# Kernel tuning notes

Hardware: AMD Instinct MI355X
Metric: run time of the kernel (lower is better)

## Reference

```python
import jax, jax.numpy as jnp
import numpy as np
import math

EPS = 1.1920929e-07  # torch.finfo(float32).eps, used by nn.RMSNorm(eps=None)

def rmsnorm(x, w):
    return x * jax.lax.rsqrt(jnp.mean(x * x, axis=-1, keepdims=True) + EPS) * w

def sinkhorn(logits, iters=20):
    m = jnp.exp(logits - logits.max(axis=-1, keepdims=True))
    def body(_, m):
        m = m / (m.sum(axis=-1, keepdims=True) + 1e-6)
        return m / (m.sum(axis=-2, keepdims=True) + 1e-6)
    return jax.lax.fori_loop(0, iters, body, m)

def ngram_hash(ids, mults):
    # ids [B,T] int32, mults [2,2,3] int32 -> [B,T,4]
    B, T = ids.shape
    padded = jnp.pad(ids, ((0, 0), (2, 0)))
    windows = jnp.stack([padded[:, k:k + T] for k in range(3)], axis=-1)  # [B,T,3]
    out = []
    for n_idx in range(2):
        L = n_idx + 2
        grams = windows[:, :, 3 - L:]                                     # [B,T,L]
        mixed = grams[:, :, None, :] * mults[n_idx, :, :L][None, None]    # [B,T,2,L]
        h = mixed[..., 0]
        for k in range(1, L):
            h = jnp.bitwise_xor(h, mixed[..., k])
        out.append(h % 4096)
    return jnp.concatenate(out, axis=2)

def short_conv(x, conv_w, norm_w):
    # depthwise causal conv, kernel 4: torch pads 3 both sides then slices [..., :T]
    B, T, G, C = x.shape
    xn = rmsnorm(x, norm_w).reshape(B, T, G * C).transpose(0, 2, 1)  # [B,GC,T]
    y = jax.lax.conv_general_dilated(xn, conv_w, (1,), [(3, 0)],
                                     feature_group_count=G * C,
                                     dimension_numbers=('NCH', 'OIH', 'NCH'))
    return jax.nn.silu(y).transpose(0, 2, 1).reshape(B, T, G, C)

def engram(x, ids, mults, emb_table, val_w, val_b, key_w, key_b, nq_w, nk_w, conv_w, convnorm_w):
    B, T = ids.shape
    hash_ids = ngram_hash(ids, mults) + jnp.array([0, 4096, 8192, 12288], dtype=jnp.int32)
    emb = emb_table[hash_ids].reshape(B, T, -1)                       # [B,T,256]
    v_base = emb @ val_w + val_b                                      # [B,T,128]
    k = rmsnorm(jnp.einsum('btd,sdc->btsc', emb, key_w) + key_b, nk_w)  # [B,T,4,128]
    q = rmsnorm(x, nq_w)
    gates = jax.nn.sigmoid(jnp.sum(q * k, axis=-1, keepdims=True) / math.sqrt(128.0))
    v_gated = v_base[:, :, None, :] * gates                           # [B,T,4,128]
    return v_gated + short_conv(v_gated, conv_w, convnorm_w)

def causal_attn(x, qkv_w, qkv_b, proj_w, proj_b):
    B, T, C = x.shape
    H, D = 4, C // 4
    q, k, v = jnp.split(x @ qkv_w + qkv_b, 3, axis=-1)
    q = q.reshape(B, T, H, D).transpose(0, 2, 1, 3)
    k = k.reshape(B, T, H, D).transpose(0, 2, 1, 3)
    v = v.reshape(B, T, H, D).transpose(0, 2, 1, 3)
    att = jnp.einsum('bhtd,bhsd->bhts', q, k) / math.sqrt(D)
    att = jnp.where(jnp.tril(jnp.ones((T, T), bool)), att, -jnp.inf)
    att = jax.nn.softmax(att, axis=-1)
    y = jnp.einsum('bhts,bhsd->bhtd', att, v).transpose(0, 2, 1, 3).reshape(B, T, C)
    return y @ proj_w + proj_b

def mhc(x, layer_fn, coef_w, pre_w, pre_b, post_w, post_b, res_w, res_b, a_pre, a_post, a_res, ln_w):
    B, T, n, C = x.shape
    xn = rmsnorm(x.reshape(B * T, n * C), coef_w)
    H_pre = jax.nn.sigmoid(a_pre * (xn @ pre_w + pre_b))             # [BT,n]
    H_post = 2.0 * jax.nn.sigmoid(a_post * (xn @ post_w + post_b))   # [BT,n]
    H_res = sinkhorn((a_res * (xn @ res_w + res_b)).reshape(-1, n, n))
    xp = x.reshape(B * T, n, C)
    x_agg = jnp.einsum('bn,bnc->bc', H_pre, xp)
    y = layer_fn(rmsnorm(x_agg.reshape(B, T, C), ln_w)).reshape(B * T, C)
    # faithful to torch einsum 'bjn,bc->bnc' applied to H_post.transpose(1,2) [BT,n,1]:
    # the stream dim j is CONTRACTED, leaving a size-1 dim that broadcasts over streams
    x_branch = H_post.sum(axis=-1)[:, None, None] * y[:, None, :]    # [BT,1,C]
    x_highway = jnp.einsum('bnm,bmc->bnc', H_res, xp)                # [BT,n,C]
    return (x_highway + x_branch).reshape(B, T, n, C)

def _forward(x, input_ids, eng_multipliers, eng_embedding, eng_val_w, eng_val_b, eng_key_w, eng_key_b, eng_nq_w, eng_nk_w, eng_conv_w, eng_convnorm_w, a_coef_w, a_pre_w, a_pre_b, a_post_w, a_post_b, a_res_w, a_res_b, a_alpha_pre, a_alpha_post, a_alpha_res, a_ln_w, qkv_w, qkv_b, attnproj_w, attnproj_b, m_coef_w, m_pre_w, m_pre_b, m_post_w, m_post_b, m_res_w, m_res_b, m_alpha_pre, m_alpha_post, m_alpha_res, m_ln_w, mlp_w1, mlp_b1, mlp_w2, mlp_b2):
    x = x + engram(x, input_ids, eng_multipliers, eng_embedding, eng_val_w, eng_val_b, eng_key_w, eng_key_b, eng_nq_w, eng_nk_w, eng_conv_w, eng_convnorm_w)
    attn_fn = lambda z: causal_attn(z, qkv_w, qkv_b, attnproj_w, attnproj_b)
    x = mhc(x, attn_fn, a_coef_w, a_pre_w, a_pre_b, a_post_w, a_post_b, a_res_w, a_res_b, a_alpha_pre, a_alpha_post, a_alpha_res, a_ln_w)
    mlp_fn = lambda z: jax.nn.silu(z @ mlp_w1 + mlp_b1) @ mlp_w2 + mlp_b2
    x = mhc(x, mlp_fn, m_coef_w, m_pre_w, m_pre_b, m_post_w, m_post_b, m_res_w, m_res_b, m_alpha_pre, m_alpha_post, m_alpha_res, m_ln_w)
    return x

def setup_inputs():
    key = jax.random.key(0)
    B, T = 256, 128
    def rnd(i, shp, scale=0.02):
        return jax.random.normal(jax.random.fold_in(key, i), shp, jnp.float32) * scale
    alpha = jnp.asarray(0.01, jnp.float32)
    return {
        'x': rnd(0, (B, T, 4, 128), 1.0),
        'input_ids': jax.random.randint(jax.random.fold_in(key, 1), (B, T), 0, 4096, jnp.int32),
        'eng_multipliers': jax.random.randint(jax.random.fold_in(key, 2), (2, 2, 3), 1, 10000, jnp.int32),
        'eng_embedding': rnd(3, (16384, 64)),
        'eng_val_w': rnd(4, (256, 128)), 'eng_val_b': jnp.zeros(128, jnp.float32),
        'eng_key_w': rnd(5, (4, 256, 128)), 'eng_key_b': jnp.zeros((4, 128), jnp.float32),
        'eng_nq_w': jnp.ones((4, 128), jnp.float32), 'eng_nk_w': jnp.ones((4, 128), jnp.float32),
        'eng_conv_w': rnd(6, (512, 1, 4), 0.1), 'eng_convnorm_w': jnp.ones((4, 128), jnp.float32),
        'a_coef_w': jnp.ones(512, jnp.float32),
        'a_pre_w': rnd(7, (512, 4)), 'a_pre_b': jnp.zeros(4, jnp.float32),
        'a_post_w': rnd(8, (512, 4)), 'a_post_b': jnp.zeros(4, jnp.float32),
        'a_res_w': rnd(9, (512, 16)), 'a_res_b': jnp.zeros(16, jnp.float32),
        'a_alpha_pre': alpha, 'a_alpha_post': alpha, 'a_alpha_res': alpha,
        'a_ln_w': jnp.ones(128, jnp.float32),
        'qkv_w': rnd(10, (128, 384)), 'qkv_b': jnp.zeros(384, jnp.float32),
        'attnproj_w': rnd(11, (128, 128)), 'attnproj_b': jnp.zeros(128, jnp.float32),
        'm_coef_w': jnp.ones(512, jnp.float32),
        'm_pre_w': rnd(12, (512, 4)), 'm_pre_b': jnp.zeros(4, jnp.float32),
        'm_post_w': rnd(13, (512, 4)), 'm_post_b': jnp.zeros(4, jnp.float32),
        'm_res_w': rnd(14, (512, 16)), 'm_res_b': jnp.zeros(16, jnp.float32),
        'm_alpha_pre': alpha, 'm_alpha_post': alpha, 'm_alpha_res': alpha,
        'm_ln_w': jnp.ones(128, jnp.float32),
        'mlp_w1': rnd(15, (128, 512)), 'mlp_b1': jnp.zeros(512, jnp.float32),
        'mlp_w2': rnd(16, (512, 128)), 'mlp_b2': jnp.zeros(128, jnp.float32),
    }

def reference(x, input_ids, eng_multipliers, eng_embedding, eng_val_w, eng_val_b, eng_key_w, eng_key_b, eng_nq_w, eng_nk_w, eng_conv_w, eng_convnorm_w, a_coef_w, a_pre_w, a_pre_b, a_post_w, a_post_b, a_res_w, a_res_b, a_alpha_pre, a_alpha_post, a_alpha_res, a_ln_w, qkv_w, qkv_b, attnproj_w, attnproj_b, m_coef_w, m_pre_w, m_pre_b, m_post_w, m_post_b, m_res_w, m_res_b, m_alpha_pre, m_alpha_post, m_alpha_res, m_ln_w, mlp_w1, mlp_b1, mlp_w2, mlp_b2):
    return _forward(x, input_ids, eng_multipliers, eng_embedding, eng_val_w, eng_val_b, eng_key_w, eng_key_b, eng_nq_w, eng_nk_w, eng_conv_w, eng_convnorm_w, a_coef_w, a_pre_w, a_pre_b, a_post_w, a_post_b, a_res_w, a_res_b, a_alpha_pre, a_alpha_post, a_alpha_res, a_ln_w, qkv_w, qkv_b, attnproj_w, attnproj_b, m_coef_w, m_pre_w, m_pre_b, m_post_w, m_post_b, m_res_w, m_res_b, m_alpha_pre, m_alpha_post, m_alpha_res, m_ln_w, mlp_w1, mlp_b1, mlp_w2, mlp_b2)
```

## Files before the change

kernel.cpp:

```cpp
#include <hip/hip_runtime.h>

#define BT 32768
#define TSEQ 128

constexpr float EPSF = 1.1920929e-07f;

typedef __attribute__((ext_vector_type(8))) short bf16x8;
typedef __attribute__((ext_vector_type(4))) float f32x4;

__device__ __forceinline__ float sigm(float z) { return 1.f / (1.f + __expf(-z)); }

__device__ __forceinline__ short bf16c(float f) {
  union { float f; unsigned u; } v; v.f = f;
  unsigned r = v.u + 0x7FFFu + ((v.u >> 16) & 1u);
  return (short)(r >> 16);
}
__device__ __forceinline__ float bf2f(short s) {
  union { unsigned u; float f; } v; v.u = ((unsigned)(unsigned short)s) << 16;
  return v.f;
}

__device__ __forceinline__ float red64(float v) {
  v += __shfl_xor(v, 1);  v += __shfl_xor(v, 2);  v += __shfl_xor(v, 4);
  v += __shfl_xor(v, 8);  v += __shfl_xor(v, 16); v += __shfl_xor(v, 32);
  return v;
}
__device__ __forceinline__ float red32(float v) {
  v += __shfl_xor(v, 1); v += __shfl_xor(v, 2); v += __shfl_xor(v, 4);
  v += __shfl_xor(v, 8); v += __shfl_xor(v, 16);
  return v;
}
__device__ __forceinline__ float red16(float v) {
  v += __shfl_xor(v, 1); v += __shfl_xor(v, 2); v += __shfl_xor(v, 4); v += __shfl_xor(v, 8);
  return v;
}
__device__ __forceinline__ float redmax16(float v) {
  v = fmaxf(v, __shfl_xor(v, 1)); v = fmaxf(v, __shfl_xor(v, 2));
  v = fmaxf(v, __shfl_xor(v, 4)); v = fmaxf(v, __shfl_xor(v, 8));
  return v;
}
__device__ __forceinline__ void load8(float* d, const float* p) {
  const float4 a = *reinterpret_cast<const float4*>(p);
  const float4 b = *reinterpret_cast<const float4*>(p + 4);
  d[0]=a.x; d[1]=a.y; d[2]=a.z; d[3]=a.w; d[4]=b.x; d[5]=b.y; d[6]=b.z; d[7]=b.w;
}

__global__ __launch_bounds__(256) void prep(
    const float* __restrict__ qkv_w, const float* __restrict__ proj_w,
    const float* __restrict__ mlp_w1, const float* __restrict__ mlp_w2,
    const float* __restrict__ val_w, const float* __restrict__ key_w,
    const float* __restrict__ a_res_w, const float* __restrict__ a_pre_w,
    const float* __restrict__ a_post_w,
    const float* __restrict__ m_res_w, const float* __restrict__ m_pre_w,
    const float* __restrict__ m_post_w,
    const float* __restrict__ a_res_b, const float* __restrict__ a_pre_b,
    const float* __restrict__ a_post_b,
    const float* __restrict__ m_res_b, const float* __restrict__ m_pre_b,
    const float* __restrict__ m_post_b,
    short* __restrict__ wt_qkv, short* __restrict__ wt_proj,
    short* __restrict__ wt_mlp1, short* __restrict__ wt_mlp2,
    short* __restrict__ wt_eng, short* __restrict__ wpk_a,
    short* __restrict__ wpk_m, float* __restrict__ bpk_a,
    float* __restrict__ bpk_m)
{
  const int idx = blockIdx.x * 256 + threadIdx.x;
  if (idx < 49152) {
    const int n = idx >> 7, k = idx & 127;
    wt_qkv[idx] = bf16c(qkv_w[k * 384 + n]);
  } else if (idx < 65536) {
    const int j = idx - 49152; const int n = j >> 7, k = j & 127;
    wt_proj[j] = bf16c(proj_w[k * 128 + n]);
  } else if (idx < 131072) {
    const int j = idx - 65536; const int n = j >> 7, k = j & 127;
    wt_mlp1[j] = bf16c(mlp_w1[k * 512 + n]);
  } else if (idx < 196608) {
    const int j = idx - 131072; const int n = j >> 9, k = j & 511;
    wt_mlp2[j] = bf16c(mlp_w2[k * 128 + n]);
  } else if (idx < 360448) {
    const int j = idx - 196608; const int n = j >> 8, k = j & 255;
    float v;
    if (n < 128) v = val_w[k * 128 + n];
    else v = key_w[(size_t)((n - 128) >> 7) * 32768 + k * 128 + (n & 127)];
    wt_eng[j] = bf16c(v);
  } else if (idx < 376832) {
    const int j = idx - 360448; const int r = j >> 9, k = j & 511;
    float v = 0.f;
    if (r < 16) v = a_res_w[k * 16 + r];
    else if (r < 20) v = a_pre_w[k * 4 + (r - 16)];
    else if (r < 24) v = a_post_w[k * 4 + (r - 20)];
    wpk_a[j] = bf16c(v);
  } else if (idx < 393216) {
    const int j = idx - 376832; const int r = j >> 9, k = j & 511;
    float v = 0.f;
    if (r < 16) v = m_res_w[k * 16 + r];
    else if (r < 20) v = m_pre_w[k * 4 + (r - 16)];
    else if (r < 24) v = m_post_w[k * 4 + (r - 20)];
    wpk_m[j] = bf16c(v);
  } else if (idx < 393280) {
    const int j = idx - 393216;
    if (j < 32) {
      float v = 0.f;
      if (j < 16) v = a_res_b[j];
      else if (j < 20) v = a_pre_b[j - 16];
      else if (j < 24) v = a_post_b[j - 20];
      bpk_a[j] = v;
    } else {
      const int r = j - 32;
      float v = 0.f;
      if (r < 16) v = m_res_b[r];
      else if (r < 20) v = m_pre_b[r - 16];
      else if (r < 24) v = m_post_b[r - 20];
      bpk_m[r] = v;
    }
  }
}

__global__ __launch_bounds__(256) void mgemm32(
    const unsigned short* __restrict__ Ab, const int lda,
    const short* __restrict__ WT, const float* __restrict__ bias,
    float* __restrict__ out, const int K,
    const float* __restrict__ rinv, const float* __restrict__ csc)
{
  __shared__ short As[64 * 64];
  __shared__ short Bs[32 * 64];
  const int tid = threadIdx.x;
  const int i0 = blockIdx.x * 64;
  const int w = tid >> 6, l = tid & 63;
  const int wm = w >> 1, wn = w & 1;
  const int kg = l >> 4, lr = l & 15;
  f32x4 acc[2];
  acc[0] = {0.f, 0.f, 0.f, 0.f};
  acc[1] = {0.f, 0.f, 0.f, 0.f};

  for (int kc = 0; kc < K; kc += 64) {
    __syncthreads();
#pragma unroll
    for (int p = 0; p < 2; ++p) {
      const int idx = p * 256 + tid;
      const int r = idx >> 3, ko = idx & 7;
      const bf16x8 v = *reinterpret_cast<const bf16x8*>(Ab + (size_t)(i0 + r) * lda + kc + ko * 8);
      const float rs = rinv[i0 + r];
      const float4 ca = *reinterpret_cast<const float4*>(csc + kc + ko * 8);
      const float4 cb = *reinterpret_cast<const float4*>(csc + kc + ko * 8 + 4);
      bf16x8 o;
      o[0] = bf16c(bf2f(v[0]) * rs * ca.x);
      o[1] = bf16c(bf2f(v[1]) * rs * ca.y);
      o[2] = bf16c(bf2f(v[2]) * rs * ca.z);
      o[3] = bf16c(bf2f(v[3]) * rs * ca.w);
      o[4] = bf16c(bf2f(v[4]) * rs * cb.x);
      o[5] = bf16c(bf2f(v[5]) * rs * cb.y);
      o[6] = bf16c(bf2f(v[6]) * rs * cb.z);
      o[7] = bf16c(bf2f(v[7]) * rs * cb.w);
      *reinterpret_cast<bf16x8*>(&As[r * 64 + ((ko ^ (r & 7)) << 3)]) = o;
    }
    {
      const int r = tid >> 3, slb = tid & 7;
      const bf16x8 v = *reinterpret_cast<const bf16x8*>(WT + (size_t)r * K + kc + slb * 8);
      *reinterpret_cast<bf16x8*>(&Bs[r * 64 + ((slb ^ (r & 7)) << 3)]) = v;
    }
    __syncthreads();
#pragma unroll
    for (int ks = 0; ks < 2; ++ks) {
      const int slot = ks * 4 + kg;
      bf16x8 af[2], bft;
#pragma unroll
      for (int mi = 0; mi < 2; ++mi) {
        const int r = wm * 32 + mi * 16 + lr;
        af[mi] = *reinterpret_cast<const bf16x8*>(&As[r * 64 + ((slot ^ (r & 7)) << 3)]);
      }
      {
        const int rb = wn * 16 + lr;
        bft = *reinterpret_cast<const bf16x8*>(&Bs[rb * 64 + ((slot ^ (rb & 7)) << 3)]);
      }
#pragma unroll
      for (int mi = 0; mi < 2; ++mi)
        acc[mi] = __builtin_amdgcn_mfma_f32_16x16x32_bf16(af[mi], bft, acc[mi], 0, 0, 0);
    }
  }
#pragma unroll
  for (int mi = 0; mi < 2; ++mi) {
    const int col = wn * 16 + lr;
    const float bv = bias[col];
#pragma unroll
    for (int j = 0; j < 4; ++j) {
      const int row = i0 + wm * 32 + mi * 16 + kg * 4 + j;
      out[(size_t)row * 32 + col] = acc[mi][j] + bv;
    }
  }
}

__global__ __launch_bounds__(256) void eng_mgemm(
    const int* __restrict__ ids, const int* __restrict__ mults,
    const float* __restrict__ table, const float* __restrict__ val_b,
    const short* __restrict__ wt_eng,
    float* __restrict__ vbase, unsigned short* __restrict__ krawb)
{
  __shared__ int hid[128][4];
  __shared__ short As[128 * 64];
  __shared__ short Bs[128 * 64];
  const int tid = threadIdx.x;
  const int i0 = blockIdx.x * 128;
  const int by = blockIdx.y;
  const int c0 = by * 128;
#pragma unroll
  for (int p = 0; p < 2; ++p) {
    const int idx = tid + p * 256;
    const int r = idx >> 2, wh = idx & 3;
    const int i = i0 + r;
    const int b = i >> 7, tt = i & 127;
    const int* __restrict__ row = ids + b * TSEQ;
    const int g2 = row[tt];
    const int g1 = (tt >= 1) ? row[tt - 1] : 0;
    const int g0 = (tt >= 2) ? row[tt - 2] : 0;
    int h;
    if (wh == 0)      h = ((g1 * mults[0]) ^ (g2 * mults[1])) & 4095;
    else if (wh == 1) h = (((g1 * mults[3]) ^ (g2 * mults[4])) & 4095) + 4096;
    else if (wh == 2) h = (((g0 * mults[6]) ^ (g1 * mults[7]) ^ (g2 * mults[8])) & 4095) + 8192;
    else              h = (((g0 * mults[9]) ^ (g1 * mults[10]) ^ (g2 * mults[11])) & 4095) + 12288;
    hid[r][wh] = h;
  }
  const int w = tid >> 6, l = tid & 63;
  const int wr = (w >> 1) * 64, wc = (w & 1) * 64;
  f32x4 acc[4][4];
#pragma unroll
  for (int mi = 0; mi < 4; ++mi)
#pragma unroll
    for (int ni = 0; ni < 4; ++ni) acc[mi][ni] = {0.f, 0.f, 0.f, 0.f};

  const int c4 = tid & 15;
  const int asl = c4 >> 1, ahf = c4 & 1;
  const int bsl = tid & 7;

  for (int kc = 0; kc < 256; kc += 64) {
    const int seg = kc >> 6;
    __syncthreads();
#pragma unroll
    for (int p = 0; p < 8; ++p) {
      const int r = (tid >> 4) + p * 16;
      const float4 v = *reinterpret_cast<const float4*>(table + (size_t)hid[r][seg] * 64 + c4 * 4);
      short4 b4; b4.x = bf16c(v.x); b4.y = bf16c(v.y); b4.z = bf16c(v.z); b4.w = bf16c(v.w);
      *reinterpret_cast<short4*>(&As[r * 64 + ((asl ^ (r & 7)) << 3) + (ahf << 2)]) = b4;
    }
#pragma unroll
    for (int p = 0; p < 4; ++p) {
      const int r = (tid >> 3) + p * 32;
      const bf16x8 v = *reinterpret_cast<const bf16x8*>(wt_eng + (size_t)(c0 + r) * 256 + kc + bsl * 8);
      *reinterpret_cast<bf16x8*>(&Bs[r * 64 + ((bsl ^ (r & 7)) << 3)]) = v;
    }
    __syncthreads();
    const int kg = l >> 4, lr = l & 15;
#pragma unroll
    for (int ks = 0; ks < 2; ++ks) {
      const int slot = ks * 4 + kg;
      bf16x8 af[4], bft[4];
#pragma unroll
      for (int mi = 0; mi < 4; ++mi) {
        const int r = wr + mi * 16 + lr;
        af[mi] = *reinterpret_cast<const bf16x8*>(&As[r * 64 + ((slot ^ (r & 7)) << 3)]);
      }
#pragma unroll
      for (int ni = 0; ni < 4; ++ni) {
        const int r = wc + ni * 16 + lr;
        bft[ni] = *reinterpret_cast<const bf16x8*>(&Bs[r * 64 + ((slot ^ (r & 7)) << 3)]);
      }
#pragma unroll
      for (int mi = 0; mi < 4; ++mi)
#pragma unroll
        for (int ni = 0; ni < 4; ++ni)
          acc[mi][ni] = __builtin_amdgcn_mfma_f32_16x16x32_bf16(af[mi], bft[ni], acc[mi][ni], 0, 0, 0);
    }
  }
  const int lr = l & 15, hi = l >> 4;
#pragma unroll
  for (int mi = 0; mi < 4; ++mi)
#pragma unroll
    for (int ni = 0; ni < 4; ++ni) {
      const int col = wc + ni * 16 + lr;
#pragma unroll
      for (int j = 0; j < 4; ++j) {
        const int row = i0 + wr + mi * 16 + hi * 4 + j;
        if (by == 0)
          vbase[(size_t)row * 128 + col] = acc[mi][ni][j] + val_b[col];
        else
          krawb[(size_t)row * 512 + (by - 1) * 128 + col] =
              (unsigned short)bf16c(acc[mi][ni][j]);
      }
    }
}

__global__ __launch_bounds__(256) void fused_gateconv(
    const unsigned short* __restrict__ krawb, const float* __restrict__ x,
    const float* __restrict__ vbase, const float* __restrict__ key_b,
    const float* __restrict__ nk_w, const float* __restrict__ nq_w,
    const float* __restrict__ conv_w, const float* __restrict__ cnw,
    unsigned short* __restrict__ xout, float* __restrict__ invout)
{
  __shared__ float vb[19 * 128];
  __shared__ float gA[19][4];
  __shared__ float gG[19][4];
  const int tid = threadIdx.x;
  const size_t rowbase = (size_t)blockIdx.x * 16;
  const int tt0 = (int)(rowbase & 127);
#pragma unroll
  for (int p = 0; p < 3; ++p) {
    const int idx = p * 256 + tid;
    if (idx < 608) {
      const int hs = idx >> 5, c4 = (idx & 31) << 2;
      float4 v = make_float4(0.f, 0.f, 0.f, 0.f);
      if (tt0 - 3 + hs >= 0)
        v = *reinterpret_cast<const float4*>(vbase + (rowbase - 3 + hs) * 128 + c4);
      *reinterpret_cast<float4*>(&vb[hs * 128 + c4]) = v;
    }
  }
  __syncthreads();
  const int w = tid >> 6, l = tid & 63;
  {
    const int s = l >> 4, li = l & 15, c0 = li * 8, j0 = l * 8;
    float kb[8], nk[8], nq[8];
    load8(kb, key_b + s * 128 + c0);
    load8(nk, nk_w + s * 128 + c0);
    load8(nq, nq_w + s * 128 + c0);
    for (int it = 0; it < 5; ++it) {
      const int ht = it * 4 + w;
      if (ht >= 19) break;
      const int tt = tt0 - 3 + ht;
      if (tt < 0) {
        if (li == 0) { gG[ht][s] = 0.f; gA[ht][s] = 0.f; }
        continue;
      }
      const size_t rg = rowbase - 3 + ht;
      float kv[8], xv[8];
      {
        const bf16x8 kvb = *reinterpret_cast<const bf16x8*>(krawb + rg * 512 + j0);
#pragma unroll
        for (int jj = 0; jj < 8; ++jj) kv[jj] = bf2f(kvb[jj]);
      }
      load8(xv, x + rg * 512 + j0);
      float ssk = 0.f, ssx = 0.f;
#pragma unroll
      for (int jj = 0; jj < 8; ++jj) {
        kv[jj] += kb[jj];
        ssk = fmaf(kv[jj], kv[jj], ssk);
        ssx = fmaf(xv[jj], xv[jj], ssx);
      }
      ssk = red16(ssk);
      ssx = red16(ssx);
      const float invk = rsqrtf(ssk * (1.f / 128.f) + EPSF);
      const float invq = rsqrtf(ssx * (1.f / 128.f) + EPSF);
      float dot = 0.f;
#pragma unroll
      for (int jj = 0; jj < 8; ++jj)
        dot = fmaf(kv[jj] * invk * nk[jj], xv[jj] * invq * nq[jj], dot);
      dot = red16(dot);
      const float gate = sigm(dot * 0.08838834764831843f);
      const float2 vb2 = *reinterpret_cast<const float2*>(&vb[ht * 128 + l * 2]);
      float ssv = vb2.x * vb2.x + vb2.y * vb2.y;
      ssv = red64(ssv);
      const float A = gate * rsqrtf(gate * gate * (ssv * (1.f / 128.f)) + EPSF);
      if (li == 0) { gG[ht][s] = gate; gA[ht][s] = A; }
    }
  }
  __syncthreads();
  {
    const int tg = tid >> 5;
    const int c4l = tid & 31;
    const int cf = c4l * 4;
    for (int ti = 0; ti < 2; ++ti) {
      const int t = tg + ti * 8;
      const size_t rg = rowbase + t;
      float ssq = 0.f;
#pragma unroll
      for (int sj = 0; sj < 4; ++sj) {
        const int j = sj * 128 + cf;
        float4 cwe[4];
#pragma unroll
        for (int e = 0; e < 4; ++e)
          cwe[e] = *reinterpret_cast<const float4*>(conv_w + (size_t)(j + e) * 4);
        const float4 cn4 = *reinterpret_cast<const float4*>(cnw + j);
        float4 vbt[4]; float av[4];
#pragma unroll
        for (int kk = 0; kk < 4; ++kk) {
          vbt[kk] = *reinterpret_cast<const float4*>(&vb[(t + kk) * 128 + cf]);
          av[kk] = gA[t + kk][sj];
        }
        const float gg = gG[t + 3][sj];
        float4 accv;
        accv.x = vbt[0].x*av[0]*cwe[0].x + vbt[1].x*av[1]*cwe[0].y + vbt[2].x*av[2]*cwe[0].z + vbt[3].x*av[3]*cwe[0].w;
        accv.y = vbt[0].y*av[0]*cwe[1].x + vbt[1].y*av[1]*cwe[1].y + vbt[2].y*av[2]*cwe[1].z + vbt[3].y*av[3]*cwe[1].w;
        accv.z = vbt[0].z*av[0]*cwe[2].x + vbt[1].z*av[1]*cwe[2].y + vbt[2].z*av[2]*cwe[2].z + vbt[3].z*av[3]*cwe[2].w;
        accv.w = vbt[0].w*av[0]*cwe[3].x + vbt[1].w*av[1]*cwe[3].y + vbt[2].w*av[2]*cwe[3].z + vbt[3].w*av[3]*cwe[3].w;
        const float4 x4 = *reinterpret_cast<const float4*>(x + rg * 512 + j);
        const float y0 = accv.x * cn4.x, y1 = accv.y * cn4.y;
        const float y2 = accv.z * cn4.z, y3 = accv.w * cn4.w;
        float4 o;
        o.x = x4.x + vbt[3].x * gg + y0 * sigm(y0);
        o.y = x4.y + vbt[3].y * gg + y1 * sigm(y1);
        o.z = x4.z + vbt[3].z * gg + y2 * sigm(y2);
        o.w = x4.w + vbt[3].w * gg + y3 * sigm(y3);
        ushort4 ob;
        ob.x = (unsigned short)bf16c(o.x);
        ob.y = (unsigned short)bf16c(o.y);
        ob.z = (unsigned short)bf16c(o.z);
        ob.w = (unsigned short)bf16c(o.w);
        *reinterpret_cast<ushort4*>(xout + rg * 512 + j) = ob;
        ssq += o.x*o.x + o.y*o.y + o.z*o.z + o.w*o.w;
      }
      ssq = red32(ssq);
      if (c4l == 0) invout[rg] = rsqrtf(ssq * (1.f / 512.f) + EPSF);
    }
  }
}

__global__ __launch_bounds__(256) void mhc_sink2(
    const float* __restrict__ proj, const unsigned short* __restrict__ xin,
    const float* __restrict__ p_apre, const float* __restrict__ p_apost,
    const float* __restrict__ p_ares, const float* __restrict__ ln_w,
    unsigned short* __restrict__ xab, float* __restrict__ hres,
    float* __restrict__ hps)
{
  const int tid = threadIdx.x;
  const int l = tid & 63;
  const size_t i = (size_t)blockIdx.x * 4 + (tid >> 6);
  const float pv = proj[i * 32 + (l & 31)];
  const float apre = p_apre[0], apost = p_apost[0], ares = p_ares[0];
  const int n = l >> 4;
  const float hp = sigm(apre * __shfl(pv, 16 + n));
  float hsum = 0.f;
#pragma unroll
  for (int t2 = 0; t2 < 4; ++t2) hsum += 2.f * sigm(apost * __shfl(pv, 20 + t2));
  const float v = ares * pv;
  float rm = fmaxf(v, __shfl_xor(v, 1));
  rm = fmaxf(rm, __shfl_xor(rm, 2));
  float m = __expf(v - rm);
#pragma unroll
  for (int it = 0; it < 20; ++it) {
    float rs = m + __shfl_xor(m, 1);
    rs += __shfl_xor(rs, 2);
    m *= __builtin_amdgcn_rcpf(rs + 1e-6f);
    float cs = m + __shfl_xor(m, 4);
    cs += __shfl_xor(cs, 8);
    m *= __builtin_amdgcn_rcpf(cs + 1e-6f);
  }
  if (l < 16) hres[i * 16 + l] = m;
  if (l == 0) hps[i] = hsum;
  const int j0 = l * 8;
  float xv[8];
  {
    const bf16x8 xb = *reinterpret_cast<const bf16x8*>(xin + i * 512 + j0);
#pragma unroll
    for (int jj = 0; jj < 8; ++jj) xv[jj] = bf2f(xb[jj]);
  }
  float ag[8];
#pragma unroll
  for (int jj = 0; jj < 8; ++jj) {
    float a2 = hp * xv[jj];
    a2 += __shfl_xor(a2, 16);
    a2 += __shfl_xor(a2, 32);
    ag[jj] = a2;
  }
  float ssa = 0.f;
#pragma unroll
  for (int jj = 0; jj < 8; ++jj) ssa = fmaf(ag[jj], ag[jj], ssa);
  ssa = red16(ssa);
  const float inva = rsqrtf(ssa * (1.f / 128.f) + EPSF);
  if (l < 16) {
    float lnw[8];
    load8(lnw, ln_w + l * 8);
    bf16x8 o;
#pragma unroll
    for (int jj = 0; jj < 8; ++jj) o[jj] = bf16c(ag[jj] * inva * lnw[jj]);
    *reinterpret_cast<bf16x8*>(xab + i * 128 + l * 8) = o;
  }
}

template <int NT, int ACT>
__global__ __launch_bounds__(256) void mgemm_bf16A(
    const unsigned short* __restrict__ Ab, const short* __restrict__ WT,
    const float* __restrict__ bias, unsigned short* __restrict__ outp)
{
  __shared__ short As[128 * 64];
  __shared__ short Bs[128 * 64];
  const int tid = threadIdx.x;
  const int i0 = blockIdx.x * 128;
  const int c0 = blockIdx.y * 128;
  const int w = tid >> 6, l = tid & 63;
  const int wr = (w >> 1) * 64, wc = (w & 1) * 64;
  const int kg = l >> 4, lr = l & 15;
  f32x4 acc[4][4];
#pragma unroll
  for (int mi = 0; mi < 4; ++mi)
#pragma unroll
    for (int ni = 0; ni < 4; ++ni) acc[mi][ni] = {0.f, 0.f, 0.f, 0.f};

#pragma unroll
  for (int kc = 0; kc < 2; ++kc) {
    __syncthreads();
#pragma unroll
    for (int p = 0; p < 4; ++p) {
      const int idx = p * 256 + tid;
      const int r = idx >> 3, slb = idx & 7;
      const bf16x8 v = *reinterpret_cast<const bf16x8*>(Ab + (size_t)(i0 + r) * 128 + kc * 64 + slb * 8);
      *reinterpret_cast<bf16x8*>(&As[r * 64 + ((slb ^ (r & 7)) << 3)]) = v;
    }
#pragma unroll
    for (int p = 0; p < 4; ++p) {
      const int idx = p * 256 + tid;
      const int r = idx >> 3, slb = idx & 7;
      const bf16x8 v = *reinterpret_cast<const bf16x8*>(WT + (size_t)(c0 + r) * 128 + kc * 64 + slb * 8);
      *reinterpret_cast<bf16x8*>(&Bs[r * 64 + ((slb ^ (r & 7)) << 3)]) = v;
    }
    __syncthreads();
#pragma unroll
    for (int ks = 0; ks < 2; ++ks) {
      const int slot = ks * 4 + kg;
      bf16x8 af[4], bft[4];
#pragma unroll
      for (int mi = 0; mi < 4; ++mi) {
        const int r = wr + mi * 16 + lr;
        af[mi] = *reinterpret_cast<const bf16x8*>(&As[r * 64 + ((slot ^ (r & 7)) << 3)]);
      }
#pragma unroll
      for (int ni = 0; ni < 4; ++ni) {
        const int r = wc + ni * 16 + lr;
        bft[ni] = *reinterpret_cast<const bf16x8*>(&Bs[r * 64 + ((slot ^ (r & 7)) << 3)]);
      }
#pragma unroll
      for (int mi = 0; mi < 4; ++mi)
#pragma unroll
        for (int ni = 0; ni < 4; ++ni)
          acc[mi][ni] = __builtin_amdgcn_mfma_f32_16x16x32_bf16(af[mi], bft[ni], acc[mi][ni], 0, 0, 0);
    }
  }
#pragma unroll
  for (int mi = 0; mi < 4; ++mi)
#pragma unroll
    for (int ni = 0; ni < 4; ++ni) {
      const int col = c0 + wc + ni * 16 + lr;
      const float bv = bias[col];
#pragma unroll
      for (int j = 0; j < 4; ++j) {
        const int row = i0 + wr + mi * 16 + kg * 4 + j;
        float o = acc[mi][ni][j] + bv;
        if (ACT == 1) o = o * sigm(o);
        outp[(size_t)row * (NT * 128) + col] = (unsigned short)bf16c(o);
      }
    }
}

template <int KT, bool WITH_INV, bool OUTBF>
__global__ __launch_bounds__(512) void gemm_combine(
    const unsigned short* __restrict__ Ab, const int lda,
    const short* __restrict__ WT, const float* __restrict__ bias,
    const unsigned short* __restrict__ xst, const float* __restrict__ hres,
    const float* __restrict__ hps, void* __restrict__ outp,
    float* __restrict__ invout)
{
  __shared__ short As[64 * 64];
  __shared__ short Bs[128 * 64];
  __shared__ short yl[64 * 132];
  __shared__ float prt[64][2];
  const int tid = threadIdx.x;
  const size_t i0 = (size_t)blockIdx.x * 64;
  const int w = tid >> 6, l = tid & 63;
  const int wm = w >> 2, wn = w & 3;
  const int kg = l >> 4, lr = l & 15;
  f32x4 acc[2][2];
#pragma unroll
  for (int mi = 0; mi < 2; ++mi)
#pragma unroll
    for (int ni = 0; ni < 2; ++ni) acc[mi][ni] = {0.f, 0.f, 0.f, 0.f};
#pragma unroll
  for (int kc = 0; kc < KT; ++kc) {
    __syncthreads();
    {
      const int r = tid >> 3, slb = tid & 7;
      const bf16x8 v = *reinterpret_cast<const bf16x8*>(Ab + (i0 + r) * lda + kc * 64 + slb * 8);
      *reinterpret_cast<bf16x8*>(&As[r * 64 + ((slb ^ (r & 7)) << 3)]) = v;
    }
#pragma unroll
    for (int p = 0; p < 2; ++p) {
      const int idx = p * 512 + tid;
      const int r = idx >> 3, slb = idx & 7;
      const bf16x8 v = *reinterpret_cast<const bf16x8*>(
          WT + (size_t)r * (KT * 64) + kc * 64 + slb * 8);
      *reinterpret_cast<bf16x8*>(&Bs[r * 64 + ((slb ^ (r & 7)) << 3)]) = v;
    }
    __syncthreads();
#pragma unroll
    for (int ks = 0; ks < 2; ++ks) {
      const int slot = ks * 4 + kg;
      bf16x8 af[2], bft[2];
#pragma unroll
      for (int mi = 0; mi < 2; ++mi) {
        const int r = wm * 32 + mi * 16 + lr;
        af[mi] = *reinterpret_cast<const bf16x8*>(&As[r * 64 + ((slot ^ (r & 7)) << 3)]);
      }
#pragma unroll
      for (int ni = 0; ni < 2; ++ni) {
        const int rb = wn * 32 + ni * 16 + lr;
        bft[ni] = *reinterpret_cast<const bf16x8*>(&Bs[rb * 64 + ((slot ^ (rb & 7)) << 3)]);
      }
#pragma unroll
      for (int mi = 0; mi < 2; ++mi)
#pragma unroll
        for (int ni = 0; ni < 2; ++ni)
          acc[mi][ni] = __builtin_amdgcn_mfma_f32_16x16x32_bf16(af[mi], bft[ni], acc[mi][ni], 0, 0, 0);
    }
  }
#pragma unroll
  for (int mi = 0; mi < 2; ++mi)
#pragma unroll
    for (int ni = 0; ni < 2; ++ni) {
      const int col = wn * 32 + ni * 16 + lr;
      const float bv = bias[col];
#pragma unroll
      for (int j = 0; j < 4; ++j) {
        const int row = wm * 32 + mi * 16 + kg * 4 + j;
        yl[row * 132 + col] = bf16c(acc[mi][ni][j] + bv);
      }
    }
  __syncthreads();
  const int c = tid & 127, tl = tid >> 7;
  for (int k = 0; k < 16; ++k) {
    const int t = tl * 16 + k;
    const size_t rg = i0 + t;
    float hv[16];
#pragma unroll
    for (int n16 = 0; n16 < 16; ++n16) hv[n16] = hres[rg * 16 + n16];
    const float g = hps[rg];
    const float yv = bf2f(yl[t * 132 + c]) * g;
    float xm[4];
#pragma unroll
    for (int m = 0; m < 4; ++m) xm[m] = bf2f((short)xst[rg * 512 + m * 128 + c]);
    float ssq = 0.f;
#pragma unroll
    for (int n = 0; n < 4; ++n) {
      const float o = hv[n*4+0]*xm[0] + hv[n*4+1]*xm[1] + hv[n*4+2]*xm[2] + hv[n*4+3]*xm[3] + yv;
      if (OUTBF)
        ((unsigned short*)outp)[rg * 512 + n * 128 + c] = (unsigned short)bf16c(o);
      else
        ((float*)outp)[rg * 512 + n * 128 + c] = o;
      if (WITH_INV) ssq = fmaf(o, o, ssq);
    }
    if (WITH_INV) {
      ssq = red64(ssq);
      if (l == 0) prt[t][(tid >> 6) & 1] = ssq;
    }
  }
  if (WITH_INV) {
    __syncthreads();
    if (tid < 64)
      invout[i0 + tid] = rsqrtf((prt[tid][0] + prt[tid][1]) * (1.f / 512.f) + EPSF);
  }
}

__global__ __launch_bounds__(256) void attn_mfma(
    const unsigned short* __restrict__ qkv, unsigned short* __restrict__ y)
{
  __shared__ short Ks[128 * 32];
  __shared__ short Vt[32 * 128];
  __shared__ short Ps[4][32 * 128];
  const int tid = threadIdx.x;
  const int b = blockIdx.x >> 2, h = blockIdx.x & 3;
  const unsigned short* __restrict__ base = qkv + (size_t)b * 128 * 384 + h * 32;
#pragma unroll
  for (int p = 0; p < 2; ++p) {
    const int idx = tid + p * 256;
    const int s = idx >> 2, c8 = idx & 3;
    const bf16x8 v = *reinterpret_cast<const bf16x8*>(base + (size_t)s * 384 + 128 + c8 * 8);
    const int chunk = c8 ^ ((s >> 1) & 3);
    *reinterpret_cast<bf16x8*>(&Ks[s * 32 + chunk * 8]) = v;
  }
#pragma unroll
  for (int p = 0; p < 4; ++p) {
    const int idx = tid + p * 256;
    const int s = idx >> 3, c4 = idx & 7;
    const ushort4 v = *reinterpret_cast<const ushort4*>(base + (size_t)s * 384 + 256 + c4 * 4);
    const int schunk = s >> 3, soff = s & 7;
#pragma unroll
    for (int k = 0; k < 4; ++k) {
      const int d = c4 * 4 + k;
      const unsigned short vv = (k == 0) ? v.x : (k == 1) ? v.y : (k == 2) ? v.z : v.w;
      Vt[d * 128 + ((schunk ^ (d & 7)) << 3) + soff] = (short)vv;
    }
  }
  const int w = tid >> 6, l = tid & 63;
  const int g = l >> 4, lr = l & 15;
  bf16x8 qa[2];
#pragma unroll
  for (int mi = 0; mi < 2; ++mi) {
    const int row = w * 32 + mi * 16 + lr;
    qa[mi] = *reinterpret_cast<const bf16x8*>(base + (size_t)row * 384 + g * 8);
  }
  __syncthreads();
  const int ntmax = 2 * w + 1;
  bf16x8 ka[8];
#pragma unroll
  for (int nt = 0; nt < 8; ++nt)
    if (nt <= ntmax) {
      const int s = nt * 16 + lr;
      const int chunk = g ^ ((s >> 1) & 3);
      ka[nt] = *reinterpret_cast<const bf16x8*>(&Ks[s * 32 + chunk * 8]);
    }
  f32x4 sacc[2][8];
#pragma unroll
  for (int mi = 0; mi < 2; ++mi)
#pragma unroll
    for (int nt = 0; nt < 8; ++nt) sacc[mi][nt] = {0.f, 0.f, 0.f, 0.f};
#pragma unroll
  for (int mi = 0; mi < 2; ++mi)
#pragma unroll
    for (int nt = 0; nt < 8; ++nt)
      if (nt <= ntmax)
        sacc[mi][nt] = __builtin_amdgcn_mfma_f32_16x16x32_bf16(qa[mi], ka[nt], sacc[mi][nt], 0, 0, 0);
  const float scl = 0.17677669529663687f;
  float rv[2][4];
  short* const pw = Ps[w];
#pragma unroll
  for (int mi = 0; mi < 2; ++mi) {
#pragma unroll
    for (int j = 0; j < 4; ++j) {
      const int row = w * 32 + mi * 16 + g * 4 + j;
      float mx = -3.4e38f;
#pragma unroll
      for (int nt = 0; nt < 8; ++nt)
        if (nt <= ntmax) {
          const int col = nt * 16 + lr;
          const float val = sacc[mi][nt][j] * scl;
          if (col <= row) mx = fmaxf(mx, val);
        }
      mx = redmax16(mx);
      float sum = 0.f;
      const int rl = mi * 16 + g * 4 + j;
#pragma unroll
      for (int nt = 0; nt < 8; ++nt)
        if (nt <= ntmax) {
          const int col = nt * 16 + lr;
          const float val = sacc[mi][nt][j] * scl;
          const float pv = (col <= row) ? __expf(val - mx) : 0.f;
          sum += pv;
          const int chunk = (2 * nt + (lr >> 3)) ^ (rl & 7);
          pw[rl * 128 + chunk * 8 + (lr & 7)] = bf16c(pv);
        }
      sum = red16(sum);
      rv[mi][j] = 1.f / sum;
    }
  }
  f32x4 oacc[2][2];
#pragma unroll
  for (int mi = 0; mi < 2; ++mi)
#pragma unroll
    for (int nt = 0; nt < 2; ++nt) oacc[mi][nt] = {0.f, 0.f, 0.f, 0.f};
#pragma unroll
  for (int kt = 0; kt < 4; ++kt)
    if (kt <= w) {
      bf16x8 pa[2], va[2];
#pragma unroll
      for (int mi = 0; mi < 2; ++mi) {
        const int rl = mi * 16 + lr;
        const int chunk = (4 * kt + g) ^ (rl & 7);
        pa[mi] = *reinterpret_cast<const bf16x8*>(&pw[rl * 128 + chunk * 8]);
      }
#pragma unroll
      for (int nt = 0; nt < 2; ++nt) {
        const int d = nt * 16 + lr;
        const int chunk = (4 * kt + g) ^ (d & 7);
        va[nt] = *reinterpret_cast<const bf16x8*>(&Vt[d * 128 + chunk * 8]);
      }
#pragma unroll
      for (int mi = 0; mi < 2; ++mi)
#pragma unroll
        for (int nt = 0; nt < 2; ++nt)
          oacc[mi][nt] = __builtin_amdgcn_mfma_f32_16x16x32_bf16(pa[mi], va[nt], oacc[mi][nt], 0, 0, 0);
    }
#pragma unroll
  for (int mi = 0; mi < 2; ++mi)
#pragma unroll
    for (int nt = 0; nt < 2; ++nt)
#pragma unroll
      for (int j = 0; j < 4; ++j) {
        const int row = w * 32 + mi * 16 + g * 4 + j;
        y[((size_t)b * 128 + row) * 128 + h * 32 + nt * 16 + lr] =
            (unsigned short)bf16c(oacc[mi][nt][j] * rv[mi][j]);
      }
}

extern "C" void kernel_launch(void* const* d_in, const int* in_sizes, int n_in,
                              void* d_out, int out_size, void* d_ws, size_t ws_size,
                              hipStream_t stream)
{
  const float* x        = (const float*)d_in[0];
  const int*   ids      = (const int*)d_in[1];
  const int*   mults    = (const int*)d_in[2];
  const float* table    = (const float*)d_in[3];
  const float* val_w    = (const float*)d_in[4];
  const float* val_b    = (const float*)d_in[5];
  const float* key_w    = (const float*)d_in[6];
  const float* key_b    = (const float*)d_in[7];
  const float* nq_w     = (const float*)d_in[8];
  const float* nk_w     = (const float*)d_in[9];
  const float* conv_w   = (const float*)d_in[10];
  const float* cnw      = (const float*)d_in[11];
  const float* a_coef   = (const float*)d_in[12];
  const float* a_pre_w  = (const float*)d_in[13];
  const float* a_pre_b  = (const float*)d_in[14];
  const float* a_post_w = (const float*)d_in[15];
  const float* a_post_b = (const float*)d_in[16];
  const float* a_res_w  = (const float*)d_in[17];
  const float* a_res_b  = (const float*)d_in[18];
  const float* a_apre   = (const float*)d_in[19];
  const float* a_apost  = (const float*)d_in[20];
  const float* a_ares   = (const float*)d_in[21];
  const float* a_ln_w   = (const float*)d_in[22];
  const float* qkv_w    = (const float*)d_in[23];
  const float* qkv_b    = (const float*)d_in[24];
  const float* proj_w   = (const float*)d_in[25];
  const float* proj_b   = (const float*)d_in[26];
  const float* m_coef   = (const float*)d_in[27];
  const float* m_pre_w  = (const float*)d_in[28];
  const float* m_pre_b  = (const float*)d_in[29];
  const float* m_post_w = (const float*)d_in[30];
  const float* m_post_b = (const float*)d_in[31];
  const float* m_res_w  = (const float*)d_in[32];
  const float* m_res_b  = (const float*)d_in[33];
  const float* m_apre   = (const float*)d_in[34];
  const float* m_apost  = (const float*)d_in[35];
  const float* m_ares   = (const float*)d_in[36];
  const float* m_ln_w   = (const float*)d_in[37];
  const float* mlp_w1   = (const float*)d_in[38];
  const float* mlp_b1   = (const float*)d_in[39];
  const float* mlp_w2   = (const float*)d_in[40];
  const float* mlp_b2   = (const float*)d_in[41];

  float* out = (float*)d_out;
  float* ws  = (float*)d_ws;
  float* vbase  = ws;
  float* proj24 = vbase + (size_t)BT * 128;
  float* hresb  = proj24 + (size_t)BT * 32;
  float* hpsb   = hresb + (size_t)BT * 16;
  float* inv1   = hpsb + (size_t)BT;
  float* inv2   = inv1 + (size_t)BT;
  float* bpk_a  = inv2 + (size_t)BT;
  float* bpk_m  = bpk_a + 32;
  short* wt_qkv  = (short*)(bpk_m + 32);
  short* wt_proj = wt_qkv  + 49152;
  short* wt_mlp1 = wt_proj + 16384;
  short* wt_mlp2 = wt_mlp1 + 65536;
  short* wt_eng  = wt_mlp2 + 65536;
  short* wpk_a   = wt_eng  + 163840;
  short* wpk_m   = wpk_a   + 16384;
  unsigned short* xab = (unsigned short*)(wpk_m + 16384);
  unsigned short* big = xab + (size_t)BT * 128;
  unsigned short* x1b = big + (size_t)BT * 512;
  unsigned short* x2b = x1b + (size_t)BT * 512;
  unsigned short* y1b = xab;

  prep<<<1537, 256, 0, stream>>>(qkv_w, proj_w, mlp_w1, mlp_w2, val_w, key_w,
                                 a_res_w, a_pre_w, a_post_w, m_res_w, m_pre_w, m_post_w,
                                 a_res_b, a_pre_b, a_post_b, m_res_b, m_pre_b, m_post_b,
                                 wt_qkv, wt_proj, wt_mlp1, wt_mlp2, wt_eng,
                                 wpk_a, wpk_m, bpk_a, bpk_m);

  eng_mgemm<<<dim3(BT / 128, 5), 256, 0, stream>>>(ids, mults, table, val_b, wt_eng,
                                                   vbase, big);
  fused_gateconv<<<BT / 16, 256, 0, stream>>>(big, x, vbase, key_b, nk_w, nq_w,
                                              conv_w, cnw, x1b, inv1);

  mgemm32<<<BT / 64, 256, 0, stream>>>(x1b, 512, wpk_a, bpk_a, proj24, 512, inv1, a_coef);
  mhc_sink2<<<BT / 4, 256, 0, stream>>>(proj24, x1b, a_apre, a_apost, a_ares, a_ln_w,
                                        xab, hresb, hpsb);
  mgemm_bf16A<3, 0><<<dim3(BT / 128, 3), 256, 0, stream>>>(xab, wt_qkv, qkv_b, big);
  attn_mfma<<<1024, 256, 0, stream>>>(big, y1b);
  gemm_combine<2, true, true><<<BT / 64, 512, 0, stream>>>(
      y1b, 128, wt_proj, proj_b, x1b, hresb, hpsb, (void*)x2b, inv2);

  mgemm32<<<BT / 64, 256, 0, stream>>>(x2b, 512, wpk_m, bpk_m, proj24, 512, inv2, m_coef);
  mhc_sink2<<<BT / 4, 256, 0, stream>>>(proj24, x2b, m_apre, m_apost, m_ares, m_ln_w,
                                        xab, hresb, hpsb);
  mgemm_bf16A<4, 1><<<dim3(BT / 128, 4), 256, 0, stream>>>(xab, wt_mlp1, mlp_b1, big);
  gemm_combine<8, false, false><<<BT / 64, 512, 0, stream>>>(
      big, 512, wt_mlp2, mlp_b2, x2b, hresb, hpsb, (void*)out, nullptr);

  (void)in_sizes; (void)n_in; (void)out_size; (void)ws_size;
}
```

Before: 290.8 us.

## Pre-convert embedding table to bf16, rebalance gate loop, stage hres in LDS

The embedding table is converted to bf16 once in the prep kernel, so eng_mgemm gathers 16-byte bf16 rows instead of converting fp32 float4 loads on every tile. The fused gate/conv kernel now assigns four lanes per (row, stream) and processes four rows per wave, so the loop runs two iterations instead of five. It pays for this by reloading krawb, x and the bias vectors a second time. gemm_combine stages the hres and hps coefficients in shared memory instead of reading them per thread from global memory. The prep launch grows to cover about one million extra table elements each call.

```diff
diff --git a/kernel.cpp b/kernel.cpp
--- a/kernel.cpp
+++ b/kernel.cpp
@@ -34,6 +34,10 @@
   v += __shfl_xor(v, 1); v += __shfl_xor(v, 2); v += __shfl_xor(v, 4); v += __shfl_xor(v, 8);
   return v;
 }
+__device__ __forceinline__ float red4(float v) {
+  v += __shfl_xor(v, 1); v += __shfl_xor(v, 2);
+  return v;
+}
 __device__ __forceinline__ float redmax16(float v) {
   v = fmaxf(v, __shfl_xor(v, 1)); v = fmaxf(v, __shfl_xor(v, 2));
   v = fmaxf(v, __shfl_xor(v, 4)); v = fmaxf(v, __shfl_xor(v, 8));
@@ -49,6 +53,7 @@
     const float* __restrict__ qkv_w, const float* __restrict__ proj_w,
     const float* __restrict__ mlp_w1, const float* __restrict__ mlp_w2,
     const float* __restrict__ val_w, const float* __restrict__ key_w,
+    const float* __restrict__ table,
     const float* __restrict__ a_res_w, const float* __restrict__ a_pre_w,
     const float* __restrict__ a_post_w,
     const float* __restrict__ m_res_w, const float* __restrict__ m_pre_w,
@@ -61,7 +66,7 @@
     short* __restrict__ wt_mlp1, short* __restrict__ wt_mlp2,
     short* __restrict__ wt_eng, short* __restrict__ wpk_a,
     short* __restrict__ wpk_m, float* __restrict__ bpk_a,
-    float* __restrict__ bpk_m)
+    float* __restrict__ bpk_m, unsigned short* __restrict__ tableb)
 {
   const int idx = blockIdx.x * 256 + threadIdx.x;
   if (idx < 49152) {
@@ -112,6 +117,9 @@
       else if (r < 24) v = m_post_b[r - 20];
       bpk_m[r] = v;
     }
+  } else if (idx < 393280 + 1048576) {
+    const int j = idx - 393280;
+    tableb[j] = (unsigned short)bf16c(table[j]);
   }
 }
 
@@ -191,7 +199,7 @@
 
 __global__ __launch_bounds__(256) void eng_mgemm(
     const int* __restrict__ ids, const int* __restrict__ mults,
-    const float* __restrict__ table, const float* __restrict__ val_b,
+    const unsigned short* __restrict__ tableb, const float* __restrict__ val_b,
     const short* __restrict__ wt_eng,
     float* __restrict__ vbase, unsigned short* __restrict__ krawb)
 {
@@ -227,19 +235,17 @@
 #pragma unroll
     for (int ni = 0; ni < 4; ++ni) acc[mi][ni] = {0.f, 0.f, 0.f, 0.f};
 
-  const int c4 = tid & 15;
-  const int asl = c4 >> 1, ahf = c4 & 1;
   const int bsl = tid & 7;
 
   for (int kc = 0; kc < 256; kc += 64) {
     const int seg = kc >> 6;
     __syncthreads();
 #pragma unroll
-    for (int p = 0; p < 8; ++p) {
-      const int r = (tid >> 4) + p * 16;
-      const float4 v = *reinterpret_cast<const float4*>(table + (size_t)hid[r][seg] * 64 + c4 * 4);
-      short4 b4; b4.x = bf16c(v.x); b4.y = bf16c(v.y); b4.z = bf16c(v.z); b4.w = bf16c(v.w);
-      *reinterpret_cast<short4*>(&As[r * 64 + ((asl ^ (r & 7)) << 3) + (ahf << 2)]) = b4;
+    for (int p = 0; p < 4; ++p) {
+      const int idx = p * 256 + tid;
+      const int r = idx >> 3, ko = idx & 7;
+      const bf16x8 v = *reinterpret_cast<const bf16x8*>(tableb + (size_t)hid[r][seg] * 64 + ko * 8);
+      *reinterpret_cast<bf16x8*>(&As[r * 64 + ((ko ^ (r & 7)) << 3)]) = v;
     }
 #pragma unroll
     for (int p = 0; p < 4; ++p) {
@@ -315,49 +321,67 @@
   __syncthreads();
   const int w = tid >> 6, l = tid & 63;
   {
-    const int s = l >> 4, li = l & 15, c0 = li * 8, j0 = l * 8;
-    float kb[8], nk[8], nq[8];
-    load8(kb, key_b + s * 128 + c0);
-    load8(nk, nk_w + s * 128 + c0);
-    load8(nq, nq_w + s * 128 + c0);
-    for (int it = 0; it < 5; ++it) {
-      const int ht = it * 4 + w;
-      if (ht >= 19) break;
-      const int tt = tt0 - 3 + ht;
-      if (tt < 0) {
-        if (li == 0) { gG[ht][s] = 0.f; gA[ht][s] = 0.f; }
-        continue;
-      }
-      const size_t rg = rowbase - 3 + ht;
-      float kv[8], xv[8];
-      {
-        const bf16x8 kvb = *reinterpret_cast<const bf16x8*>(krawb + rg * 512 + j0);
-#pragma unroll
-        for (int jj = 0; jj < 8; ++jj) kv[jj] = bf2f(kvb[jj]);
-      }
-      load8(xv, x + rg * 512 + j0);
-      float ssk = 0.f, ssx = 0.f;
-#pragma unroll
-      for (int jj = 0; jj < 8; ++jj) {
-        kv[jj] += kb[jj];
-        ssk = fmaf(kv[jj], kv[jj], ssk);
-        ssx = fmaf(xv[jj], xv[jj], ssx);
-      }
-      ssk = red16(ssk);
-      ssx = red16(ssx);
-      const float invk = rsqrtf(ssk * (1.f / 128.f) + EPSF);
-      const float invq = rsqrtf(ssx * (1.f / 128.f) + EPSF);
-      float dot = 0.f;
-#pragma unroll
-      for (int jj = 0; jj < 8; ++jj)
-        dot = fmaf(kv[jj] * invk * nk[jj], xv[jj] * invq * nq[jj], dot);
-      dot = red16(dot);
-      const float gate = sigm(dot * 0.08838834764831843f);
-      const float2 vb2 = *reinterpret_cast<const float2*>(&vb[ht * 128 + l * 2]);
-      float ssv = vb2.x * vb2.x + vb2.y * vb2.y;
-      ssv = red64(ssv);
-      const float A = gate * rsqrtf(gate * gate * (ssv * (1.f / 128.f)) + EPSF);
-      if (li == 0) { gG[ht][s] = gate; gA[ht][s] = A; }
+    const int tk = l >> 4;
+    const int li = l & 15;
+    const int s = li >> 2;
+    const int cb = s * 128 + (li & 3) * 32;
+    for (int it = 0; it < 2; ++it) {
+      const int ht = it * 16 + w * 4 + tk;
+      if (ht < 19) {
+        const int tt = tt0 - 3 + ht;
+        if (tt < 0) {
+          if ((li & 3) == 0) { gG[ht][s] = 0.f; gA[ht][s] = 0.f; }
+        } else {
+          const size_t rg = rowbase - 3 + ht;
+          float ssk = 0.f, ssx = 0.f;
+#pragma unroll
+          for (int ch = 0; ch < 4; ++ch) {
+            const int o = cb + ch * 8;
+            const bf16x8 kvb = *reinterpret_cast<const bf16x8*>(krawb + rg * 512 + o);
+            float kb8[8], x8[8];
+            load8(kb8, key_b + o);
+            load8(x8, x + rg * 512 + o);
+#pragma unroll
+            for (int jj = 0; jj < 8; ++jj) {
+              const float kvf = bf2f(kvb[jj]) + kb8[jj];
+              ssk = fmaf(kvf, kvf, ssk);
+              ssx = fmaf(x8[jj], x8[jj], ssx);
+            }
+          }
+          ssk = red4(ssk);
+          ssx = red4(ssx);
+          const float invk = rsqrtf(ssk * (1.f / 128.f) + EPSF);
+          const float invq = rsqrtf(ssx * (1.f / 128.f) + EPSF);
+          float dot = 0.f;
+#pragma unroll
+          for (int ch = 0; ch < 4; ++ch) {
+            const int o = cb + ch * 8;
+            const bf16x8 kvb = *reinterpret_cast<const bf16x8*>(krawb + rg * 512 + o);
+            float kb8[8], x8[8], nk8[8], nq8[8];
+            load8(kb8, key_b + o);
+            load8(x8, x + rg * 512 + o);
+            load8(nk8, nk_w + o);
+            load8(nq8, nq_w + o);
+#pragma unroll
+            for (int jj = 0; jj < 8; ++jj) {
+              const float kvf = (bf2f(kvb[jj]) + kb8[jj]) * invk * nk8[jj];
+              dot = fmaf(kvf, x8[jj] * invq * nq8[jj], dot);
+            }
+          }
+          dot = red4(dot);
+          const float gate = sigm(dot * 0.08838834764831843f);
+          float ssv;
+          {
+            const float4 a = *reinterpret_cast<const float4*>(&vb[ht * 128 + li * 8]);
+            const float4 b = *reinterpret_cast<const float4*>(&vb[ht * 128 + li * 8 + 4]);
+            ssv = a.x*a.x + a.y*a.y + a.z*a.z + a.w*a.w
+                + b.x*b.x + b.y*b.y + b.z*b.z + b.w*b.w;
+          }
+          ssv = red16(ssv);
+          const float A = gate * rsqrtf(gate * gate * (ssv * (1.f / 128.f)) + EPSF);
+          if ((li & 3) == 0) { gG[ht][s] = gate; gA[ht][s] = A; }
+        }
+      }
     }
   }
   __syncthreads();
@@ -559,6 +583,8 @@
   __shared__ short Bs[128 * 64];
   __shared__ short yl[64 * 132];
   __shared__ float prt[64][2];
+  __shared__ float hl[64 * 16];
+  __shared__ float hpl[64];
   const int tid = threadIdx.x;
   const size_t i0 = (size_t)blockIdx.x * 64;
   const int w = tid >> 6, l = tid & 63;
@@ -619,15 +645,18 @@
         yl[row * 132 + col] = bf16c(acc[mi][ni][j] + bv);
       }
     }
+#pragma unroll
+  for (int p = 0; p < 2; ++p) {
+    const int idx = p * 512 + tid;
+    hl[idx] = hres[(i0 + (idx >> 4)) * 16 + (idx & 15)];
+  }
+  if (tid < 64) hpl[tid] = hps[i0 + tid];
   __syncthreads();
   const int c = tid & 127, tl = tid >> 7;
   for (int k = 0; k < 16; ++k) {
     const int t = tl * 16 + k;
     const size_t rg = i0 + t;
-    float hv[16];
-#pragma unroll
-    for (int n16 = 0; n16 < 16; ++n16) hv[n16] = hres[rg * 16 + n16];
-    const float g = hps[rg];
+    const float g = hpl[t];
     const float yv = bf2f(yl[t * 132 + c]) * g;
     float xm[4];
 #pragma unroll
@@ -635,7 +664,8 @@
     float ssq = 0.f;
 #pragma unroll
     for (int n = 0; n < 4; ++n) {
-      const float o = hv[n*4+0]*xm[0] + hv[n*4+1]*xm[1] + hv[n*4+2]*xm[2] + hv[n*4+3]*xm[3] + yv;
+      const float o = hl[t*16+n*4+0]*xm[0] + hl[t*16+n*4+1]*xm[1]
+                    + hl[t*16+n*4+2]*xm[2] + hl[t*16+n*4+3]*xm[3] + yv;
       if (OUTBF)
         ((unsigned short*)outp)[rg * 512 + n * 128 + c] = (unsigned short)bf16c(o);
       else
@@ -853,15 +883,16 @@
   unsigned short* big = xab + (size_t)BT * 128;
   unsigned short* x1b = big + (size_t)BT * 512;
   unsigned short* x2b = x1b + (size_t)BT * 512;
+  unsigned short* tableb = x2b + (size_t)BT * 512;
   unsigned short* y1b = xab;
 
-  prep<<<1537, 256, 0, stream>>>(qkv_w, proj_w, mlp_w1, mlp_w2, val_w, key_w,
+  prep<<<5633, 256, 0, stream>>>(qkv_w, proj_w, mlp_w1, mlp_w2, val_w, key_w, table,
                                  a_res_w, a_pre_w, a_post_w, m_res_w, m_pre_w, m_post_w,
                                  a_res_b, a_pre_b, a_post_b, m_res_b, m_pre_b, m_post_b,
                                  wt_qkv, wt_proj, wt_mlp1, wt_mlp2, wt_eng,
-                                 wpk_a, wpk_m, bpk_a, bpk_m);
-
-  eng_mgemm<<<dim3(BT / 128, 5), 256, 0, stream>>>(ids, mults, table, val_b, wt_eng,
+                                 wpk_a, wpk_m, bpk_a, bpk_m, tableb);
+
+  eng_mgemm<<<dim3(BT / 128, 5), 256, 0, stream>>>(ids, mults, tableb, val_b, wt_eng,
                                                    vbase, big);
   fused_gateconv<<<BT / 16, 256, 0, stream>>>(big, x, vbase, key_b, nk_w, nq_w,
                                               conv_w, cnw, x1b, inv1);
```

New measurement: 303.5 us. 4.4% more time.
